# Optimization experiments

Measured on AMD Instinct MI355X. Metric: run time of the kernel, lower is better.

## Reference

```python
import jax, jax.numpy as jnp
import numpy as np

N_HEAD = 16

def setup_inputs() -> dict:
    key = jax.random.key(0)
    ks = jax.random.split(key, 9)
    B, T, C = 1, 4096, 1024
    s = 1.0 / np.sqrt(C)
    x = jax.random.normal(ks[0], (B, T, C), dtype=jnp.float32)
    Wq = jax.random.uniform(ks[1], (C, C), jnp.float32, -s, s)
    bq = jax.random.uniform(ks[2], (C,), jnp.float32, -s, s)
    Wk = jax.random.uniform(ks[3], (C, C), jnp.float32, -s, s)
    bk = jax.random.uniform(ks[4], (C,), jnp.float32, -s, s)
    Wv = jax.random.uniform(ks[5], (C, C), jnp.float32, -s, s)
    bv = jax.random.uniform(ks[6], (C,), jnp.float32, -s, s)
    Wp = jax.random.uniform(ks[7], (C, C), jnp.float32, -s, s)
    bp = jax.random.uniform(ks[8], (C,), jnp.float32, -s, s)
    return {"x": x, "Wq": Wq, "bq": bq, "Wk": Wk, "bk": bk,
            "Wv": Wv, "bv": bv, "Wp": Wp, "bp": bp}

def reference(x, Wq, bq, Wk, bk, Wv, bv, Wp, bp):
    B, T, C = x.shape
    H = N_HEAD
    D = C // H
    # projections -> (B, H, T, D)
    def proj(W, b):
        return (x @ W.T + b).reshape(B, T, H, D).transpose(0, 2, 1, 3)
    q, k, v = proj(Wq, bq), proj(Wk, bk), proj(Wv, bv)
    scale = 1.0 / np.sqrt(D).astype(np.float32)
    att = jnp.einsum('bhtd,bhsd->bhts', q, k) * scale  # (B,H,T,T)
    causal = jnp.tril(jnp.ones((T, T), dtype=bool))
    att = jnp.where(causal[None, None], att, -jnp.inf)
    att = jax.nn.softmax(att, axis=-1)
    y = jnp.einsum('bhts,bhsd->bhtd', att, v)  # (B,H,T,D)
    y = y.transpose(0, 2, 1, 3).reshape(B, T, C)
    return y @ Wp.T + bp
```

## Files before the change

kernel.cpp:

```cpp
#include <hip/hip_runtime.h>
#include <hip/hip_bf16.h>
#include <math.h>

typedef __bf16 bf16x8 __attribute__((ext_vector_type(8)));
typedef __bf16 bf16x4 __attribute__((ext_vector_type(4)));
typedef float f32x4 __attribute__((ext_vector_type(4)));

#define MFMA_BF16 __builtin_amdgcn_mfma_f32_16x16x32_bf16

#define QSCALE 0.18033688011112042f

__device__ inline void async_load16(const __hip_bfloat16* g, __hip_bfloat16* l) {
    __builtin_amdgcn_global_load_lds(
        (const __attribute__((address_space(1))) unsigned int*)g,
        (__attribute__((address_space(3))) unsigned int*)l,
        16, 0, 0);
}

__device__ inline int sig(int x) {
    return (x & ~12) | ((x & 4) << 1) | ((x & 8) >> 1);
}

__device__ inline unsigned int pack_bf16_trunc(float lo, float hi) {
    return __builtin_amdgcn_perm(__float_as_uint(hi), __float_as_uint(lo),
                                 0x07060302u);
}

__global__ __launch_bounds__(256) void convert_all(
    const float* __restrict__ x,
    const float* __restrict__ Wq, const float* __restrict__ Wk,
    const float* __restrict__ Wv, const float* __restrict__ Wp,
    __hip_bfloat16* __restrict__ xb,
    __hip_bfloat16* __restrict__ Wqb, __hip_bfloat16* __restrict__ Wkb,
    __hip_bfloat16* __restrict__ Wvb, __hip_bfloat16* __restrict__ Wpb,
    int nx, int nw)
{
    const int xblocks = nx >> 11;
    const int wblocks = nw >> 11;
    int b = blockIdx.x;
    const float* in;
    __hip_bfloat16* out;
    int i;
    if (b < xblocks) {
        in = x; out = xb; i = (b * 256 + threadIdx.x) * 8;
    } else {
        b -= xblocks;
        const int w = b / wblocks, bb = b - w * wblocks;
        in  = w == 0 ? Wq : w == 1 ? Wk : w == 2 ? Wv : Wp;
        out = w == 0 ? Wqb : w == 1 ? Wkb : w == 2 ? Wvb : Wpb;
        i = (bb * 256 + threadIdx.x) * 8;
    }
    const float4 a = *(const float4*)(in + i);
    const float4 c = *(const float4*)(in + i + 4);
    __hip_bfloat16 tmp[8];
    tmp[0] = __float2bfloat16(a.x); tmp[1] = __float2bfloat16(a.y);
    tmp[2] = __float2bfloat16(a.z); tmp[3] = __float2bfloat16(a.w);
    tmp[4] = __float2bfloat16(c.x); tmp[5] = __float2bfloat16(c.y);
    tmp[6] = __float2bfloat16(c.z); tmp[7] = __float2bfloat16(c.w);
    *(bf16x8*)(out + i) = *(const bf16x8*)tmp;
}

__global__ __launch_bounds__(512) void gemm_qkv(
    const __hip_bfloat16* __restrict__ A,
    const __hip_bfloat16* __restrict__ B,
    const float* __restrict__ bq, const float* __restrict__ bk, const float* __restrict__ bv,
    __hip_bfloat16* __restrict__ Qo, __hip_bfloat16* __restrict__ Ko,
    __hip_bfloat16* __restrict__ Vt,
    int M, int K)
{
    __shared__ __align__(16) __hip_bfloat16 smem[2][2 * 128 * 64];

    const int tid  = threadIdx.x;
    const int lane = tid & 63;
    const int wave = tid >> 6;
    const int l15  = lane & 15;
    const int quad = lane >> 4;
    const int m0 = blockIdx.x * 128;
    const int n0 = blockIdx.y * 128;
    const int wr = wave >> 1;
    const int wc = wave & 1;
    const int sel = n0 >> 10;

    f32x4 acc[2][4] = {};

    int srow[2], scol[2];
    #pragma unroll
    for (int i = 0; i < 2; ++i) {
        const int c = tid + 512 * i;
        srow[i] = c >> 3;
        scol[i] = ((c & 7) ^ (srow[i] & 7)) * 8;
    }

    auto stageg = [&](int k0, int buf) {
        __hip_bfloat16* As = smem[buf];
        __hip_bfloat16* Bs = smem[buf] + 128 * 64;
        #pragma unroll
        for (int i = 0; i < 2; ++i) {
            async_load16(A + (size_t)(m0 + srow[i]) * K + k0 + scol[i],
                         As + (size_t)(tid + 512 * i) * 8);
            async_load16(B + (size_t)(n0 + srow[i]) * K + k0 + scol[i],
                         Bs + (size_t)(tid + 512 * i) * 8);
        }
    };

    const int NK = K >> 6;
    stageg(0, 0);

    for (int kt = 0; kt < NK; ++kt) {
        asm volatile("s_waitcnt vmcnt(0)\n\ts_barrier" ::: "memory");
        if (kt + 1 < NK) stageg((kt + 1) * 64, (kt + 1) & 1);

        const __hip_bfloat16* As = smem[kt & 1];
        const __hip_bfloat16* Bs = smem[kt & 1] + 128 * 64;

        #pragma unroll
        for (int kd = 0; kd < 2; ++kd) {
            bf16x8 af[2], bfr[4];
            #pragma unroll
            for (int mi = 0; mi < 2; ++mi) {
                const int row = wr * 32 + mi * 16 + l15;
                af[mi] = *(const bf16x8*)(
                    As + row * 64 + (((kd * 4 + quad) ^ (row & 7)) << 3));
            }
            #pragma unroll
            for (int ni = 0; ni < 4; ++ni) {
                const int row = wc * 64 + ni * 16 + l15;
                bfr[ni] = *(const bf16x8*)(
                    Bs + row * 64 + (((kd * 4 + quad) ^ (row & 7)) << 3));
            }
            #pragma unroll
            for (int mi = 0; mi < 2; ++mi)
                #pragma unroll
                for (int ni = 0; ni < 4; ++ni)
                    acc[mi][ni] = MFMA_BF16(af[mi], bfr[ni], acc[mi][ni], 0, 0, 0);
        }
    }

    if (sel == 2) {
        __hip_bfloat16* tsm = smem[0];
        __syncthreads();
        #pragma unroll
        for (int ni = 0; ni < 4; ++ni) {
            const int lc = wc * 64 + ni * 16 + l15;
            const float bias = bv[(n0 + lc) & 1023];
            #pragma unroll
            for (int mi = 0; mi < 2; ++mi) {
                const int mb = wr * 32 + mi * 16 + quad * 4;
                const int g = mb >> 3, off = mb & 7;
                __hip_bfloat16 t[4];
                #pragma unroll
                for (int r = 0; r < 4; ++r)
                    t[r] = __float2bfloat16(acc[mi][ni][r] + bias);
                *(bf16x4*)(tsm + lc * 128 + ((g ^ (lc & 15)) << 3) + off)
                    = *(const bf16x4*)t;
            }
        }
        __syncthreads();
        const int cc0 = n0 & 1023;
        #pragma unroll
        for (int i = 0; i < 4; ++i) {
            const int q = tid + 512 * i;
            const int ch = q >> 4, mg = q & 15;
            bf16x8 v = *(const bf16x8*)(tsm + ch * 128 + ((mg ^ (ch & 15)) << 3));
            *(bf16x8*)(Vt + (size_t)(cc0 + ch) * M + m0 + mg * 8) = v;
        }
    } else {
        __hip_bfloat16* dst = sel == 0 ? Qo : Ko;
        const float* bptr   = sel == 0 ? bq : bk;
        const float sc      = sel == 0 ? QSCALE : 1.0f;
        #pragma unroll
        for (int ni = 0; ni < 4; ++ni) {
            const int cc = (n0 + wc * 64 + ni * 16 + l15) & 1023;
            const float bias = bptr[cc];
            #pragma unroll
            for (int mi = 0; mi < 2; ++mi) {
                const int row = m0 + wr * 32 + mi * 16 + quad * 4;
                #pragma unroll
                for (int r = 0; r < 4; ++r)
                    dst[(size_t)(row + r) * 1024 + cc] =
                        __float2bfloat16((acc[mi][ni][r] + bias) * sc);
            }
        }
    }
}

__global__ __launch_bounds__(512) void gemm_out_f32(
    const __hip_bfloat16* __restrict__ A,
    const __hip_bfloat16* __restrict__ B,
    const float* __restrict__ bias,
    float* __restrict__ Cf,
    int M, int N, int K)
{
    __shared__ __align__(16) __hip_bfloat16 smem[2][2 * 128 * 64];

    const int tid  = threadIdx.x;
    const int lane = tid & 63;
    const int wave = tid >> 6;
    const int l15  = lane & 15;
    const int quad = lane >> 4;
    const int m0 = blockIdx.x * 128;
    const int n0 = blockIdx.y * 128;
    const int wr = wave >> 1;
    const int wc = wave & 1;

    f32x4 acc[2][4] = {};

    int srow[2], scol[2];
    #pragma unroll
    for (int i = 0; i < 2; ++i) {
        const int c = tid + 512 * i;
        srow[i] = c >> 3;
        scol[i] = ((c & 7) ^ (srow[i] & 7)) * 8;
    }

    auto stageg = [&](int k0, int buf) {
        __hip_bfloat16* As = smem[buf];
        __hip_bfloat16* Bs = smem[buf] + 128 * 64;
        #pragma unroll
        for (int i = 0; i < 2; ++i) {
            async_load16(A + (size_t)(m0 + srow[i]) * K + k0 + scol[i],
                         As + (size_t)(tid + 512 * i) * 8);
            async_load16(B + (size_t)(n0 + srow[i]) * K + k0 + scol[i],
                         Bs + (size_t)(tid + 512 * i) * 8);
        }
    };

    const int NK = K >> 6;
    stageg(0, 0);

    for (int kt = 0; kt < NK; ++kt) {
        asm volatile("s_waitcnt vmcnt(0)\n\ts_barrier" ::: "memory");
        if (kt + 1 < NK) stageg((kt + 1) * 64, (kt + 1) & 1);

        const __hip_bfloat16* As = smem[kt & 1];
        const __hip_bfloat16* Bs = smem[kt & 1] + 128 * 64;

        #pragma unroll
        for (int kd = 0; kd < 2; ++kd) {
            bf16x8 af[2], bfr[4];
            #pragma unroll
            for (int mi = 0; mi < 2; ++mi) {
                const int row = wr * 32 + mi * 16 + l15;
                af[mi] = *(const bf16x8*)(
                    As + row * 64 + (((kd * 4 + quad) ^ (row & 7)) << 3));
            }
            #pragma unroll
            for (int ni = 0; ni < 4; ++ni) {
                const int row = wc * 64 + ni * 16 + l15;
                bfr[ni] = *(const bf16x8*)(
                    Bs + row * 64 + (((kd * 4 + quad) ^ (row & 7)) << 3));
            }
            #pragma unroll
            for (int mi = 0; mi < 2; ++mi)
                #pragma unroll
                for (int ni = 0; ni < 4; ++ni)
                    acc[mi][ni] = MFMA_BF16(af[mi], bfr[ni], acc[mi][ni], 0, 0, 0);
        }
    }

    #pragma unroll
    for (int ni = 0; ni < 4; ++ni) {
        const int col = n0 + wc * 64 + ni * 16 + l15;
        const float bv = bias[col];
        #pragma unroll
        for (int mi = 0; mi < 2; ++mi) {
            const int row = m0 + wr * 32 + mi * 16 + quad * 4;
            #pragma unroll
            for (int r = 0; r < 4; ++r)
                Cf[(size_t)(row + r) * N + col] = acc[mi][ni][r] + bv;
        }
    }
}

__global__ __launch_bounds__(512, 4) void attn_causal(
    const __hip_bfloat16* __restrict__ Q,
    const __hip_bfloat16* __restrict__ K,
    const __hip_bfloat16* __restrict__ Vt,
    __hip_bfloat16* __restrict__ PoB,
    float* __restrict__ PlB,
    int T, int C)
{
    const int nwg  = (int)(gridDim.x * gridDim.y);
    const int chunk = nwg >> 3;
    const int lin  = (int)(blockIdx.x + gridDim.x * blockIdx.y);
    const int work = (lin & 7) * chunk + (lin >> 3);
    const int h  = work >> 5;
    const int bx = work & 31;
    const int j  = bx & 7;
    const int sq = bx >> 3;
    const int tid  = threadIdx.x;
    const int w    = tid >> 6;
    const int lane = tid & 63;
    const int l15  = lane & 15;
    const int quad = lane >> 4;

    const size_t TCs = (size_t)T * C;
    const size_t HT  = (size_t)T * 16;
    __hip_bfloat16* Po = PoB + (size_t)sq * TCs;
    float* Pl = PlB + (size_t)sq * HT;

    const int len1 = j + 1, len2 = 16 - j;
    const int tile1 = j,    tile2 = 15 - j;
    const int kb1 = len1 * sq, kb2 = len2 * sq;

    __shared__ __align__(16) __hip_bfloat16 Ks[4][64 * 64];
    __shared__ __align__(16) __hip_bfloat16 Vts[4][64 * 64];

    const int r0 = tid >> 3, g0 = ((tid & 7) ^ (r0 & 7)) * 8;
    const __hip_bfloat16* Kg0 = K + (size_t)sig(r0) * C + h * 64 + g0;
    const __hip_bfloat16* Vg0 = Vt + (size_t)(h * 64 + r0) * T + g0;

    int koff[2][4], voff[2][4];
    #pragma unroll
    for (int kd = 0; kd < 2; ++kd)
        #pragma unroll
        for (int sb = 0; sb < 4; ++sb) {
            const int kappa = 32 * (sb & 1) + 8 * (l15 >> 2) + 4 * (sb >> 1) + (l15 & 3);
            const int rho = sig(kappa);
            koff[kd][sb] = rho * 64 + (((kd * 4 + quad) ^ (rho & 7)) << 3);
        }
    #pragma unroll
    for (int kk = 0; kk < 2; ++kk)
        #pragma unroll
        for (int db = 0; db < 4; ++db) {
            const int vrow = db * 16 + l15;
            voff[kk][db] = vrow * 64 + (((kk * 4 + quad) ^ (vrow & 7)) << 3);
        }

    bf16x8 ones;
    #pragma unroll
    for (int jj = 0; jj < 8; ++jj) ones[jj] = (__bf16)1.0f;

    int qbase = tile1 * 256 + w * 32;
    bf16x8 aq[2][2];
    #pragma unroll
    for (int rb = 0; rb < 2; ++rb)
        #pragma unroll
        for (int kd = 0; kd < 2; ++kd)
            aq[rb][kd] = *(const bf16x8*)(
                Q + (size_t)(qbase + rb * 16 + l15) * C + h * 64 + kd * 32 + quad * 8);

    f32x4 o[2][4] = {};
    f32x4 lacc[2] = {};

    auto stage = [&](int idx) {
        const int kb = (idx < len1) ? (kb1 + idx) : (kb2 + idx - len1);
        const size_t so = (size_t)kb << 6;
        const int sl = idx & 3;
        async_load16(Kg0 + so * C, &Ks[sl][tid * 8]);
        async_load16(Vg0 + so, &Vts[sl][tid * 8]);
    };

    stage(0);
    stage(1);

    for (int it = 0; it < 17; ++it) {
        if (it + 2 < 17) stage(it + 2);
        if (it < 15)
            asm volatile("s_waitcnt vmcnt(4)\n\ts_barrier" ::: "memory");
        else if (it == 15)
            asm volatile("s_waitcnt vmcnt(2)\n\ts_barrier" ::: "memory");
        else
            asm volatile("s_waitcnt vmcnt(0)\n\ts_barrier" ::: "memory");

        const int cur = it & 3;
        const int kb = (it < len1) ? (kb1 + it) : (kb2 + it - len1);
        const int s0 = kb << 6;

        if (it == len1) {
            #pragma unroll
            for (int rb = 0; rb < 2; ++rb) {
                const int row = qbase + rb * 16 + l15;
                #pragma unroll
                for (int db = 0; db < 4; ++db) {
                    __hip_bfloat16 t[4];
                    #pragma unroll
                    for (int r = 0; r < 4; ++r)
                        t[r] = __float2bfloat16(o[rb][db][r]);
                    *(bf16x4*)(Po + (size_t)row * C + h * 64 + db * 16 + quad * 4)
                        = *(const bf16x4*)t;
                    o[rb][db] = (f32x4){0.f, 0.f, 0.f, 0.f};
                }
                if (quad == 0)
                    Pl[(size_t)h * T + row] = lacc[rb][0];
                lacc[rb] = (f32x4){0.f, 0.f, 0.f, 0.f};
            }
            qbase = tile2 * 256 + w * 32;
            #pragma unroll
            for (int rb = 0; rb < 2; ++rb)
                #pragma unroll
                for (int kd = 0; kd < 2; ++kd)
                    aq[rb][kd] = *(const bf16x8*)(
                        Q + (size_t)(qbase + rb * 16 + l15) * C + h * 64 + kd * 32 + quad * 8);
        }

        if (s0 <= qbase + 31) {
            f32x4 sv[2][4] = {};
            #pragma unroll
            for (int kd = 0; kd < 2; ++kd)
                #pragma unroll
                for (int sb = 0; sb < 4; ++sb) {
                    bf16x8 ak = *(const bf16x8*)(&Ks[cur][koff[kd][sb]]);
                    sv[0][sb] = MFMA_BF16(ak, aq[0][kd], sv[0][sb], 0, 0, 0);
                    sv[1][sb] = MFMA_BF16(ak, aq[1][kd], sv[1][sb], 0, 0, 0);
                }

            const bool diag = (s0 + 63 > qbase);
            bf16x8 bp[2][2];
            #pragma unroll
            for (int rb = 0; rb < 2; ++rb) {
                float pv[4][4];
                #pragma unroll
                for (int sb = 0; sb < 4; ++sb)
                    #pragma unroll
                    for (int r = 0; r < 4; ++r)
                        pv[sb][r] = __builtin_amdgcn_exp2f(sv[rb][sb][r]);
                if (diag) {
                    const int thr = qbase + rb * 16 + l15 - s0 - 8 * quad;
                    #pragma unroll
                    for (int sb = 0; sb < 4; ++sb)
                        #pragma unroll
                        for (int r = 0; r < 4; ++r) {
                            const int c = 32 * (sb & 1) + 4 * (sb >> 1) + r;
                            pv[sb][r] = (c <= thr) ? pv[sb][r] : 0.f;
                        }
                }
                #pragma unroll
                for (int kk = 0; kk < 2; ++kk) {
                    union { unsigned int u[4]; bf16x8 v; } pk;
                    pk.u[0] = pack_bf16_trunc(pv[kk][0], pv[kk][1]);
                    pk.u[1] = pack_bf16_trunc(pv[kk][2], pv[kk][3]);
                    pk.u[2] = pack_bf16_trunc(pv[kk + 2][0], pv[kk + 2][1]);
                    pk.u[3] = pack_bf16_trunc(pv[kk + 2][2], pv[kk + 2][3]);
                    bp[rb][kk] = pk.v;
                }
            }

            lacc[0] = MFMA_BF16(ones, bp[0][0], lacc[0], 0, 0, 0);
            lacc[0] = MFMA_BF16(ones, bp[0][1], lacc[0], 0, 0, 0);
            lacc[1] = MFMA_BF16(ones, bp[1][0], lacc[1], 0, 0, 0);
            lacc[1] = MFMA_BF16(ones, bp[1][1], lacc[1], 0, 0, 0);

            #pragma unroll
            for (int kk = 0; kk < 2; ++kk)
                #pragma unroll
                for (int db = 0; db < 4; ++db) {
                    bf16x8 av = *(const bf16x8*)(&Vts[cur][voff[kk][db]]);
                    o[0][db] = MFMA_BF16(av, bp[0][kk], o[0][db], 0, 0, 0);
                    o[1][db] = MFMA_BF16(av, bp[1][kk], o[1][db], 0, 0, 0);
                }
        }
    }

    #pragma unroll
    for (int rb = 0; rb < 2; ++rb) {
        const int row = qbase + rb * 16 + l15;
        #pragma unroll
        for (int db = 0; db < 4; ++db) {
            __hip_bfloat16 t[4];
            #pragma unroll
            for (int r = 0; r < 4; ++r)
                t[r] = __float2bfloat16(o[rb][db][r]);
            *(bf16x4*)(Po + (size_t)row * C + h * 64 + db * 16 + quad * 4)
                = *(const bf16x4*)t;
        }
        if (quad == 0)
            Pl[(size_t)h * T + row] = lacc[rb][0];
    }
}

__global__ __launch_bounds__(256) void merge_y(
    const __hip_bfloat16* __restrict__ PoB, const float* __restrict__ PlB,
    __hip_bfloat16* __restrict__ Y, int T, int C)
{
    const size_t i = ((size_t)blockIdx.x * 256 + threadIdx.x) * 8;
    const int row = (int)(i / C);
    const int h   = ((int)(i % C)) >> 6;
    const size_t TC = (size_t)T * C;
    const size_t HT = (size_t)T * 16;
    float acc[8] = {};
    float l = 0.f;
    #pragma unroll
    for (int z = 0; z < 4; ++z) {
        bf16x8 a = *(const bf16x8*)(PoB + z * TC + i);
        #pragma unroll
        for (int r = 0; r < 8; ++r)
            acc[r] += (float)(((const __bf16*)&a)[r]);
        l += PlB[z * HT + (size_t)h * T + row];
    }
    const float inv = 1.0f / l;
    __hip_bfloat16 t[8];
    #pragma unroll
    for (int r = 0; r < 8; ++r)
        t[r] = __float2bfloat16(acc[r] * inv);
    *(bf16x8*)(Y + i) = *(const bf16x8*)t;
}

extern "C" void kernel_launch(void* const* d_in, const int* in_sizes, int n_in,
                              void* d_out, int out_size, void* d_ws, size_t ws_size,
                              hipStream_t stream)
{
    const float* x  = (const float*)d_in[0];
    const float* Wq = (const float*)d_in[1];
    const float* bq = (const float*)d_in[2];
    const float* Wk = (const float*)d_in[3];
    const float* bk = (const float*)d_in[4];
    const float* Wv = (const float*)d_in[5];
    const float* bv = (const float*)d_in[6];
    const float* Wp = (const float*)d_in[7];
    const float* bp = (const float*)d_in[8];

    const int C = 1024;
    const int T = in_sizes[0] / C;
    const int H = 16;
    const size_t TC = (size_t)T * C;
    const size_t CC = (size_t)C * C;

    __hip_bfloat16* xb  = (__hip_bfloat16*)d_ws;
    __hip_bfloat16* Wqb = xb + TC;
    __hip_bfloat16* Wkb = Wqb + CC;
    __hip_bfloat16* Wvb = Wkb + CC;
    __hip_bfloat16* Wpb = Wvb + CC;
    __hip_bfloat16* Qw  = Wpb + CC;
    __hip_bfloat16* Kw  = Qw + TC;
    __hip_bfloat16* Vtw = Kw + TC;
    __hip_bfloat16* PoB = Vtw + TC;
    float* PlB = (float*)(PoB + 4 * TC);
    __hip_bfloat16* Yw  = xb;
    float* out = (float*)d_out;

    convert_all<<<(int)(TC / 2048 + 4 * CC / 2048), 256, 0, stream>>>(
        x, Wq, Wk, Wv, Wp, xb, Wqb, Wkb, Wvb, Wpb, (int)TC, (int)CC);

    gemm_qkv<<<dim3(T / 128, 3072 / 128), 512, 0, stream>>>(
        xb, Wqb, bq, bk, bv, Qw, Kw, Vtw, T, C);

    attn_causal<<<dim3(32, H), 512, 0, stream>>>(
        Qw, Kw, Vtw, PoB, PlB, T, C);

    merge_y<<<(int)(TC / 8 / 256), 256, 0, stream>>>(
        PoB, PlB, Yw, T, C);

    gemm_out_f32<<<dim3(T / 128, C / 128), 512, 0, stream>>>(
        Yw, Wpb, bp, out, T, C, C);
}
```

Baseline: 186.0 us.

## Fuse x conversion into QKV GEMM and split-merge into output GEMM

The QKV GEMM now loads fp32 x directly into registers and converts it to bf16 before writing shared memory, so x no longer needs a separate conversion pass. The output projection GEMM reads the four partial attention outputs and their normalizers and merges them while staging its A tile, which removes the merge_y kernel and the round trip through Y. Together these drop a kernel launch and several large global read/write passes. In exchange, the A operand moves from async global-to-LDS loads to register-staged loads. QKV A-tile reads double in width, and the output GEMM re-reads the partials once per N-block (8x), which may make it memory-bound.

After: 196.9 us. 1.06x slower.

```diff
diff --git a/kernel.cpp b/kernel.cpp
--- a/kernel.cpp
+++ b/kernel.cpp
@@ -61,7 +61,7 @@
 }
 
 __global__ __launch_bounds__(512) void gemm_qkv(
-    const __hip_bfloat16* __restrict__ A,
+    const float* __restrict__ A,
     const __hip_bfloat16* __restrict__ B,
     const float* __restrict__ bq, const float* __restrict__ bk, const float* __restrict__ bv,
     __hip_bfloat16* __restrict__ Qo, __hip_bfloat16* __restrict__ Ko,
@@ -91,24 +91,45 @@
         scol[i] = ((c & 7) ^ (srow[i] & 7)) * 8;
     }
 
-    auto stageg = [&](int k0, int buf) {
+    float4 areg[4];
+    auto stageA_load = [&](int k0) {
+        #pragma unroll
+        for (int i = 0; i < 2; ++i) {
+            const float* src = A + (size_t)(m0 + srow[i]) * K + k0 + scol[i];
+            areg[2 * i]     = *(const float4*)src;
+            areg[2 * i + 1] = *(const float4*)(src + 4);
+        }
+    };
+    auto stageA_write = [&](int buf) {
         __hip_bfloat16* As = smem[buf];
+        #pragma unroll
+        for (int i = 0; i < 2; ++i) {
+            const float4 a = areg[2 * i], c4 = areg[2 * i + 1];
+            __hip_bfloat16 t[8];
+            t[0] = __float2bfloat16(a.x);  t[1] = __float2bfloat16(a.y);
+            t[2] = __float2bfloat16(a.z);  t[3] = __float2bfloat16(a.w);
+            t[4] = __float2bfloat16(c4.x); t[5] = __float2bfloat16(c4.y);
+            t[6] = __float2bfloat16(c4.z); t[7] = __float2bfloat16(c4.w);
+            *(bf16x8*)(As + (size_t)(tid + 512 * i) * 8) = *(const bf16x8*)t;
+        }
+    };
+    auto stageB = [&](int k0, int buf) {
         __hip_bfloat16* Bs = smem[buf] + 128 * 64;
         #pragma unroll
-        for (int i = 0; i < 2; ++i) {
-            async_load16(A + (size_t)(m0 + srow[i]) * K + k0 + scol[i],
-                         As + (size_t)(tid + 512 * i) * 8);
+        for (int i = 0; i < 2; ++i)
             async_load16(B + (size_t)(n0 + srow[i]) * K + k0 + scol[i],
                          Bs + (size_t)(tid + 512 * i) * 8);
-        }
     };
 
     const int NK = K >> 6;
-    stageg(0, 0);
+    stageA_load(0);
+    stageB(0, 0);
+    stageA_write(0);
 
     for (int kt = 0; kt < NK; ++kt) {
-        asm volatile("s_waitcnt vmcnt(0)\n\ts_barrier" ::: "memory");
-        if (kt + 1 < NK) stageg((kt + 1) * 64, (kt + 1) & 1);
+        asm volatile("s_waitcnt vmcnt(0) lgkmcnt(0)\n\ts_barrier" ::: "memory");
+        const bool more = kt + 1 < NK;
+        if (more) { stageA_load((kt + 1) * 64); stageB((kt + 1) * 64, (kt + 1) & 1); }
 
         const __hip_bfloat16* As = smem[kt & 1];
         const __hip_bfloat16* Bs = smem[kt & 1] + 128 * 64;
@@ -134,6 +155,8 @@
                 for (int ni = 0; ni < 4; ++ni)
                     acc[mi][ni] = MFMA_BF16(af[mi], bfr[ni], acc[mi][ni], 0, 0, 0);
         }
+
+        if (more) stageA_write((kt + 1) & 1);
     }
 
     if (sel == 2) {
@@ -185,7 +208,8 @@
 }
 
 __global__ __launch_bounds__(512) void gemm_out_f32(
-    const __hip_bfloat16* __restrict__ A,
+    const __hip_bfloat16* __restrict__ PoB,
+    const float* __restrict__ PlB,
     const __hip_bfloat16* __restrict__ B,
     const float* __restrict__ bias,
     float* __restrict__ Cf,
@@ -203,6 +227,9 @@
     const int wr = wave >> 1;
     const int wc = wave & 1;
 
+    const size_t TCs = (size_t)M * K;
+    const size_t HT  = (size_t)M * 16;
+
     f32x4 acc[2][4] = {};
 
     int srow[2], scol[2];
@@ -213,24 +240,58 @@
         scol[i] = ((c & 7) ^ (srow[i] & 7)) * 8;
     }
 
-    auto stageg = [&](int k0, int buf) {
+    bf16x8 preg[8];
+    float  lval[2];
+    auto stageA_load = [&](int k0) {
+        #pragma unroll
+        for (int i = 0; i < 2; ++i) {
+            const size_t off = (size_t)(m0 + srow[i]) * K + k0 + scol[i];
+            #pragma unroll
+            for (int z = 0; z < 4; ++z)
+                preg[4 * i + z] = *(const bf16x8*)(PoB + (size_t)z * TCs + off);
+            const int hh = (k0 + scol[i]) >> 6;
+            float l = 0.f;
+            #pragma unroll
+            for (int z = 0; z < 4; ++z)
+                l += PlB[(size_t)z * HT + (size_t)hh * M + (m0 + srow[i])];
+            lval[i] = l;
+        }
+    };
+    auto stageA_write = [&](int buf) {
         __hip_bfloat16* As = smem[buf];
+        #pragma unroll
+        for (int i = 0; i < 2; ++i) {
+            const float inv = 1.0f / lval[i];
+            float a8[8] = {};
+            #pragma unroll
+            for (int z = 0; z < 4; ++z)
+                #pragma unroll
+                for (int r = 0; r < 8; ++r)
+                    a8[r] += (float)(((const __bf16*)&preg[4 * i + z])[r]);
+            __hip_bfloat16 t[8];
+            #pragma unroll
+            for (int r = 0; r < 8; ++r)
+                t[r] = __float2bfloat16(a8[r] * inv);
+            *(bf16x8*)(As + (size_t)(tid + 512 * i) * 8) = *(const bf16x8*)t;
+        }
+    };
+    auto stageB = [&](int k0, int buf) {
         __hip_bfloat16* Bs = smem[buf] + 128 * 64;
         #pragma unroll
-        for (int i = 0; i < 2; ++i) {
-            async_load16(A + (size_t)(m0 + srow[i]) * K + k0 + scol[i],
-                         As + (size_t)(tid + 512 * i) * 8);
+        for (int i = 0; i < 2; ++i)
             async_load16(B + (size_t)(n0 + srow[i]) * K + k0 + scol[i],
                          Bs + (size_t)(tid + 512 * i) * 8);
-        }
     };
 
     const int NK = K >> 6;
-    stageg(0, 0);
+    stageA_load(0);
+    stageB(0, 0);
+    stageA_write(0);
 
     for (int kt = 0; kt < NK; ++kt) {
-        asm volatile("s_waitcnt vmcnt(0)\n\ts_barrier" ::: "memory");
-        if (kt + 1 < NK) stageg((kt + 1) * 64, (kt + 1) & 1);
+        asm volatile("s_waitcnt vmcnt(0) lgkmcnt(0)\n\ts_barrier" ::: "memory");
+        const bool more = kt + 1 < NK;
+        if (more) { stageA_load((kt + 1) * 64); stageB((kt + 1) * 64, (kt + 1) & 1); }
 
         const __hip_bfloat16* As = smem[kt & 1];
         const __hip_bfloat16* Bs = smem[kt & 1] + 128 * 64;
@@ -256,6 +317,8 @@
                 for (int ni = 0; ni < 4; ++ni)
                     acc[mi][ni] = MFMA_BF16(af[mi], bfr[ni], acc[mi][ni], 0, 0, 0);
         }
+
+        if (more) stageA_write((kt + 1) & 1);
     }
 
     #pragma unroll
@@ -469,33 +532,6 @@
     }
 }
 
-__global__ __launch_bounds__(256) void merge_y(
-    const __hip_bfloat16* __restrict__ PoB, const float* __restrict__ PlB,
-    __hip_bfloat16* __restrict__ Y, int T, int C)
-{
-    const size_t i = ((size_t)blockIdx.x * 256 + threadIdx.x) * 8;
-    const int row = (int)(i / C);
-    const int h   = ((int)(i % C)) >> 6;
-    const size_t TC = (size_t)T * C;
-    const size_t HT = (size_t)T * 16;
-    float acc[8] = {};
-    float l = 0.f;
-    #pragma unroll
-    for (int z = 0; z < 4; ++z) {
-        bf16x8 a = *(const bf16x8*)(PoB + z * TC + i);
-        #pragma unroll
-        for (int r = 0; r < 8; ++r)
-            acc[r] += (float)(((const __bf16*)&a)[r]);
-        l += PlB[z * HT + (size_t)h * T + row];
-    }
-    const float inv = 1.0f / l;
-    __hip_bfloat16 t[8];
-    #pragma unroll
-    for (int r = 0; r < 8; ++r)
-        t[r] = __float2bfloat16(acc[r] * inv);
-    *(bf16x8*)(Y + i) = *(const bf16x8*)t;
-}
-
 extern "C" void kernel_launch(void* const* d_in, const int* in_sizes, int n_in,
                               void* d_out, int out_size, void* d_ws, size_t ws_size,
                               hipStream_t stream)
@@ -526,21 +562,17 @@
     __hip_bfloat16* Vtw = Kw + TC;
     __hip_bfloat16* PoB = Vtw + TC;
     float* PlB = (float*)(PoB + 4 * TC);
-    __hip_bfloat16* Yw  = xb;
     float* out = (float*)d_out;
 
-    convert_all<<<(int)(TC / 2048 + 4 * CC / 2048), 256, 0, stream>>>(
-        x, Wq, Wk, Wv, Wp, xb, Wqb, Wkb, Wvb, Wpb, (int)TC, (int)CC);
+    convert_all<<<(int)(4 * CC / 2048), 256, 0, stream>>>(
+        x, Wq, Wk, Wv, Wp, xb, Wqb, Wkb, Wvb, Wpb, 0, (int)CC);
 
     gemm_qkv<<<dim3(T / 128, 3072 / 128), 512, 0, stream>>>(
-        xb, Wqb, bq, bk, bv, Qw, Kw, Vtw, T, C);
+        x, Wqb, bq, bk, bv, Qw, Kw, Vtw, T, C);
 
     attn_causal<<<dim3(32, H), 512, 0, stream>>>(
         Qw, Kw, Vtw, PoB, PlB, T, C);
 
-    merge_y<<<(int)(TC / 8 / 256), 256, 0, stream>>>(
-        PoB, PlB, Yw, T, C);
-
     gemm_out_f32<<<dim3(T / 128, C / 128), 512, 0, stream>>>(
-        Yw, Wpb, bp, out, T, C, C);
-}
+        PoB, PlB, Wpb, bp, out, T, C, C);
+}
```
